# Kernel optimization log

Hardware: AMD Instinct MI355X
Metric: run time of the kernel (lower is better)

The kernel has to match this reference:

```python
import jax, jax.numpy as jnp
import numpy as np

B, L, D, H = 2, 2048, 1024, 16
HD = D // H

def setup_inputs() -> dict:
    key = jax.random.key(0)
    ks = jax.random.split(key, 5)
    s = 0.02
    return {
        "x": jax.random.normal(ks[0], (B, L, D), dtype=jnp.float32),
        "Wqkv": jax.random.normal(ks[1], (D, 3 * D), dtype=jnp.float32) * s,
        "bqkv": jnp.zeros((3 * D,), dtype=jnp.float32),
        "Wproj": jax.random.normal(ks[2], (D, D), dtype=jnp.float32) * s,
        "bproj": jnp.zeros((D,), dtype=jnp.float32),
    }

def reference(x, Wqkv, bqkv, Wproj, bproj):
    b, l, d = x.shape
    scale = (d // H) ** -0.5
    qkv = x @ Wqkv + bqkv  # (B,L,3D)
    q, k, v = jnp.split(qkv, 3, axis=-1)
    # (B,H,L,hd)
    q = q.reshape(b, l, H, HD).transpose(0, 2, 1, 3)
    k = k.reshape(b, l, H, HD).transpose(0, 2, 1, 3)
    v = v.reshape(b, l, H, HD).transpose(0, 2, 1, 3)
    attn = jnp.einsum("bhqd,bhkd->bhqk", q, k) * scale
    causal = jnp.tril(jnp.ones((l, l), dtype=bool))  # True = keep
    attn = jnp.where(causal[None, None, :, :], attn, -jnp.inf)
    attn = jax.nn.softmax(attn, axis=-1)
    out = jnp.einsum("bhqk,bhkd->bhqd", attn, v)
    out = out.transpose(0, 2, 1, 3).reshape(b, l, d)
    return out @ Wproj + bproj
```

## Files before the change

kernel.cpp:

```cpp
#include <hip/hip_runtime.h>
#include <hip/hip_bf16.h>


typedef __attribute__((ext_vector_type(8))) short s16x8;
typedef __attribute__((ext_vector_type(4))) float f32x4;

__device__ __forceinline__ unsigned short f2b(float f) {
  __hip_bfloat16 h = __float2bfloat16(f);
  return *reinterpret_cast<unsigned short*>(&h);
}

__device__ __forceinline__ void gl_lds16(const void* g, void* l) {
  __builtin_amdgcn_global_load_lds(
      (const __attribute__((address_space(1))) unsigned int*)g,
      (__attribute__((address_space(3))) unsigned int*)l,
      16, 0, 0);
}


__global__ __launch_bounds__(256) void convert_f32_bf16(
    const float* __restrict__ in, unsigned short* __restrict__ out, int n4) {
  int i = blockIdx.x * 256 + threadIdx.x;
  if (i >= n4) return;
  float4 v = reinterpret_cast<const float4*>(in)[i];
  ushort4 o;
  o.x = f2b(v.x); o.y = f2b(v.y); o.z = f2b(v.z); o.w = f2b(v.w);
  reinterpret_cast<ushort4*>(out)[i] = o;
}

__global__ __launch_bounds__(256) void transpose_f32_bf16(
    const float* __restrict__ in, unsigned short* __restrict__ out, int R, int C) {
  __shared__ float tile[32][33];
  int cb = blockIdx.x * 32, rb = blockIdx.y * 32;
  int tx = threadIdx.x, ty = threadIdx.y;
  #pragma unroll
  for (int i = ty; i < 32; i += 8)
    tile[i][tx] = in[(size_t)(rb + i) * C + cb + tx];
  __syncthreads();
  #pragma unroll
  for (int i = ty; i < 32; i += 8)
    out[(size_t)(cb + i) * R + rb + tx] = f2b(tile[tx][i]);
}

__global__ __launch_bounds__(256) void transpose_v(
    const unsigned short* __restrict__ in, unsigned short* __restrict__ out) {
  __shared__ unsigned int tile[64][65];
  const int bh = blockIdx.y;
  const int l0 = blockIdx.x * 64;
  const int tx = threadIdx.x;
  const int ty = threadIdx.y;
  #pragma unroll
  for (int i = ty; i < 64; i += 4)
    tile[i][tx] = in[((size_t)bh * 2048 + l0 + i) * 64 + tx];
  __syncthreads();
  #pragma unroll
  for (int i = ty; i < 64; i += 4)
    out[((size_t)bh * 64 + i) * 2048 + l0 + tx] = (unsigned short)tile[tx][i];
}

template <int MODE>
__global__ __launch_bounds__(256) void gemm128(
    const unsigned short* __restrict__ A, const unsigned short* __restrict__ Bt,
    const float* __restrict__ bias, unsigned short* __restrict__ qOut,
    unsigned short* __restrict__ kOut, unsigned short* __restrict__ vOut,
    float* __restrict__ fOut) {
  __shared__ char sA[16384];
  __shared__ char sB[16384];
  const int tid = threadIdx.x;
  const int wid = tid >> 6, lane = tid & 63;
  const int lg = lane >> 4, lr = lane & 15;
  const int wr = wid >> 1, wc = wid & 1;
  const int nwgx = gridDim.x;
  const int id = blockIdx.y * nwgx + blockIdx.x;
  const int cpx = (nwgx * gridDim.y) >> 3;
  const int sid = (id & 7) * cpx + (id >> 3);
  const int mb = sid / nwgx, nb = sid % nwgx;

  f32x4 acc[4][4];
  #pragma unroll
  for (int i = 0; i < 4; ++i)
    #pragma unroll
    for (int j = 0; j < 4; ++j) acc[i][j] = f32x4{0.f, 0.f, 0.f, 0.f};

  for (int ks = 0; ks < 16; ++ks) {
    __syncthreads();
    #pragma unroll
    for (int r = 0; r < 4; ++r) {
      const int chunk = r * 4 + wid;
      const int o = chunk * 1024 + lane * 16;
      const int row = o >> 7;
      const int c16 = (o >> 4) & 7;
      const int swz = (c16 ^ (row & 7)) << 4;
      gl_lds16((const char*)A + ((size_t)(mb * 128 + row) * 1024 + ks * 64) * 2 + swz,
               sA + chunk * 1024);
      gl_lds16((const char*)Bt + ((size_t)(nb * 128 + row) * 1024 + ks * 64) * 2 + swz,
               sB + chunk * 1024);
    }
    __syncthreads();
    #pragma unroll
    for (int kb = 0; kb < 2; ++kb) {
      s16x8 af[4], bfr[4];
      #pragma unroll
      for (int mt = 0; mt < 4; ++mt) {
        const int rrow = wr * 64 + mt * 16 + lr;
        const int off = kb * 64 + lg * 16;
        af[mt] = *(const s16x8*)(sA + rrow * 128 + (off ^ ((rrow & 7) << 4)));
      }
      #pragma unroll
      for (int nt = 0; nt < 4; ++nt) {
        const int rrow = wc * 64 + nt * 16 + lr;
        const int off = kb * 64 + lg * 16;
        bfr[nt] = *(const s16x8*)(sB + rrow * 128 + (off ^ ((rrow & 7) << 4)));
      }
      #pragma unroll
      for (int mt = 0; mt < 4; ++mt)
        #pragma unroll
        for (int nt = 0; nt < 4; ++nt)
          acc[mt][nt] = __builtin_amdgcn_mfma_f32_16x16x32_bf16(
              af[mt], bfr[nt], acc[mt][nt], 0, 0, 0);
    }
  }

  #pragma unroll
  for (int mt = 0; mt < 4; ++mt)
    #pragma unroll
    for (int nt = 0; nt < 4; ++nt)
      #pragma unroll
      for (int r = 0; r < 4; ++r) {
        const int m = mb * 128 + wr * 64 + mt * 16 + lg * 4 + r;
        const int n = nb * 128 + wc * 64 + nt * 16 + lr;
        float val = acc[mt][nt][r] + bias[n];
        if constexpr (MODE == 0) {
          const int b = m >> 11, ml = m & 2047;
          if (n < 1024) {
            const int h = n >> 6, d = n & 63;
            qOut[((size_t)((b * 16 + h) * 2048 + ml)) * 64 + d] =
                f2b(val * 0.18033688f);
          } else if (n < 2048) {
            const int nn = n - 1024, h = nn >> 6, d = nn & 63;
            kOut[((size_t)((b * 16 + h) * 2048 + ml)) * 64 + d] = f2b(val);
          } else {
            const int nn = n - 2048, h = nn >> 6, d = nn & 63;
            vOut[((size_t)((b * 16 + h) * 2048 + ml)) * 64 + d] = f2b(val);
          }
        } else {
          fOut[(size_t)m * 1024 + n] = val;
        }
      }
}

__global__ __launch_bounds__(256, 2) void attn_fwd(
    const unsigned short* __restrict__ Q, const unsigned short* __restrict__ Kb,
    const unsigned short* __restrict__ Vt, unsigned short* __restrict__ O) {
  __shared__ char sP[16384];
  __shared__ float obuf[32 * 68];
  __shared__ float mlbuf[4][32][2];
  __shared__ float lginv[32];

  const int bid = blockIdx.x;
  const int idx = bid >> 3;
  const int bh = (bid & 7) * 4 + (idx & 3);
  const int qseg = 63 - (idx >> 2);
  const int b = bh >> 4, h = bh & 15;
  const int tid = threadIdx.x;
  const int wid = tid >> 6, lane = tid & 63;
  const int lg = lane >> 4, lr = lane & 15;
  const int base = qseg * 32;

  for (int i = tid; i < 32 * 68; i += 256) obuf[i] = 0.f;

  s16x8 qf[2][2];
  #pragma unroll
  for (int mt = 0; mt < 2; ++mt)
    #pragma unroll
    for (int kb = 0; kb < 2; ++kb) {
      const int row = base + mt * 16 + lr;
      qf[mt][kb] = *(const s16x8*)(Q + (size_t)(bh * 2048 + row) * 64 + kb * 32 + lg * 8);
    }

  f32x4 acc[2][4];
  float rm[2][4], rl[2][4];
  #pragma unroll
  for (int i = 0; i < 2; ++i)
    #pragma unroll
    for (int jj = 0; jj < 4; ++jj) {
      acc[i][jj] = f32x4{0.f, 0.f, 0.f, 0.f};
      rm[i][jj] = -INFINITY;
      rl[i][jj] = 0.f;
    }

  char* wbase = sP + wid * 4096;
  const int nkv = (qseg >> 1) + 1;

  for (int t = wid; t < nkv; t += 4) {
    const int kv0 = t * 64;

    f32x4 sfr[2][4];
    #pragma unroll
    for (int i = 0; i < 2; ++i)
      #pragma unroll
      for (int jj = 0; jj < 4; ++jj) sfr[i][jj] = f32x4{0.f, 0.f, 0.f, 0.f};
    #pragma unroll
    for (int kb = 0; kb < 2; ++kb) {
      s16x8 kf[4];
      #pragma unroll
      for (int nt = 0; nt < 4; ++nt)
        kf[nt] = *(const s16x8*)(Kb +
            (size_t)(bh * 2048 + kv0 + nt * 16 + lr) * 64 + kb * 32 + lg * 8);
      #pragma unroll
      for (int mt = 0; mt < 2; ++mt)
        #pragma unroll
        for (int nt = 0; nt < 4; ++nt)
          sfr[mt][nt] = __builtin_amdgcn_mfma_f32_16x16x32_bf16(
              qf[mt][kb], kf[nt], sfr[mt][nt], 0, 0, 0);
    }

    s16x8 vf[2][4];
    #pragma unroll
    for (int kb = 0; kb < 2; ++kb)
      #pragma unroll
      for (int nt = 0; nt < 4; ++nt)
        vf[kb][nt] = *(const s16x8*)(Vt +
            (size_t)(bh * 64 + nt * 16 + lr) * 2048 + kv0 + kb * 32 + lg * 8);

    #pragma unroll
    for (int mt = 0; mt < 2; ++mt) {
      #pragma unroll
      for (int r = 0; r < 4; ++r) {
        const int grow = base + mt * 16 + lg * 4 + r;
        float tmax = -INFINITY;
        #pragma unroll
        for (int nt = 0; nt < 4; ++nt) {
          const int col = kv0 + nt * 16 + lr;
          float s = sfr[mt][nt][r];
          if (col > grow) s = -INFINITY;
          sfr[mt][nt][r] = s;
          tmax = fmaxf(tmax, s);
        }
        tmax = fmaxf(tmax, __shfl_xor(tmax, 1));
        tmax = fmaxf(tmax, __shfl_xor(tmax, 2));
        tmax = fmaxf(tmax, __shfl_xor(tmax, 4));
        tmax = fmaxf(tmax, __shfl_xor(tmax, 8));
        const float mold = rm[mt][r];
        const float mnew = fmaxf(mold, tmax);
        const float alpha = exp2f(mold - mnew);
        float psum = 0.f;
        #pragma unroll
        for (int nt = 0; nt < 4; ++nt) {
          const float p = exp2f(sfr[mt][nt][r] - mnew);
          sfr[mt][nt][r] = p;
          psum += p;
        }
        psum += __shfl_xor(psum, 1);
        psum += __shfl_xor(psum, 2);
        psum += __shfl_xor(psum, 4);
        psum += __shfl_xor(psum, 8);
        rl[mt][r] = rl[mt][r] * alpha + psum;
        rm[mt][r] = mnew;
        #pragma unroll
        for (int nt = 0; nt < 4; ++nt) acc[mt][nt][r] *= alpha;
        const int prow = mt * 16 + lg * 4 + r;
        #pragma unroll
        for (int nt = 0; nt < 4; ++nt) {
          const int pcolb = nt * 32 + lr * 2;
          *(unsigned short*)(wbase + prow * 128 + (pcolb ^ ((prow & 7) << 4))) =
              f2b(sfr[mt][nt][r]);
        }
      }
    }

    s16x8 pf[2][2];
    #pragma unroll
    for (int mt = 0; mt < 2; ++mt)
      #pragma unroll
      for (int kb = 0; kb < 2; ++kb) {
        const int prow = mt * 16 + lr;
        const int off = kb * 64 + lg * 16;
        pf[mt][kb] = *(const s16x8*)(wbase + prow * 128 + (off ^ ((prow & 7) << 4)));
      }
    #pragma unroll
    for (int mt = 0; mt < 2; ++mt)
      #pragma unroll
      for (int nt = 0; nt < 4; ++nt)
        #pragma unroll
        for (int kb = 0; kb < 2; ++kb)
          acc[mt][nt] = __builtin_amdgcn_mfma_f32_16x16x32_bf16(
              pf[mt][kb], vf[kb][nt], acc[mt][nt], 0, 0, 0);
  }

  if (lr == 0) {
    #pragma unroll
    for (int mt = 0; mt < 2; ++mt)
      #pragma unroll
      for (int r = 0; r < 4; ++r) {
        const int row = mt * 16 + lg * 4 + r;
        mlbuf[wid][row][0] = rm[mt][r];
        mlbuf[wid][row][1] = rl[mt][r];
      }
  }
  __syncthreads();

  float beta[2][4];
  #pragma unroll
  for (int mt = 0; mt < 2; ++mt)
    #pragma unroll
    for (int r = 0; r < 4; ++r) {
      const int row = mt * 16 + lg * 4 + r;
      const float m0 = mlbuf[0][row][0], m1 = mlbuf[1][row][0];
      const float m2 = mlbuf[2][row][0], m3 = mlbuf[3][row][0];
      const float mg = fmaxf(fmaxf(m0, m1), fmaxf(m2, m3));
      const float lsum = mlbuf[0][row][1] * exp2f(m0 - mg)
                       + mlbuf[1][row][1] * exp2f(m1 - mg)
                       + mlbuf[2][row][1] * exp2f(m2 - mg)
                       + mlbuf[3][row][1] * exp2f(m3 - mg);
      beta[mt][r] = exp2f(rm[mt][r] - mg);
      if (wid == 0 && lr == 0) lginv[row] = 1.f / lsum;
    }

  #pragma unroll
  for (int w = 0; w < 4; ++w) {
    if (wid == w) {
      #pragma unroll
      for (int mt = 0; mt < 2; ++mt)
        #pragma unroll
        for (int nt = 0; nt < 4; ++nt)
          #pragma unroll
          for (int r = 0; r < 4; ++r) {
            const int row = mt * 16 + lg * 4 + r;
            const int col = nt * 16 + lr;
            obuf[row * 68 + col] += acc[mt][nt][r] * beta[mt][r];
          }
    }
    __syncthreads();
  }

  {
    const int row = (wid << 3) + (lane >> 3);
    const int c0 = (lane & 7) * 8;
    const float li = lginv[row];
    const float4 v0 = *(const float4*)&obuf[row * 68 + c0];
    const float4 v1 = *(const float4*)&obuf[row * 68 + c0 + 4];
    s16x8 o;
    o[0] = (short)f2b(v0.x * li); o[1] = (short)f2b(v0.y * li);
    o[2] = (short)f2b(v0.z * li); o[3] = (short)f2b(v0.w * li);
    o[4] = (short)f2b(v1.x * li); o[5] = (short)f2b(v1.y * li);
    o[6] = (short)f2b(v1.z * li); o[7] = (short)f2b(v1.w * li);
    const int grow = base + row;
    *(s16x8*)(O + (size_t)(b * 2048 + grow) * 1024 + h * 64 + c0) = o;
  }
}


extern "C" void kernel_launch(void* const* d_in, const int* in_sizes, int n_in,
                              void* d_out, int out_size, void* d_ws, size_t ws_size,
                              hipStream_t stream) {
  const float* x     = (const float*)d_in[0];
  const float* Wqkv  = (const float*)d_in[1];
  const float* bqkv  = (const float*)d_in[2];
  const float* Wproj = (const float*)d_in[3];
  const float* bproj = (const float*)d_in[4];
  float* out = (float*)d_out;

  char* ws = (char*)d_ws;
  unsigned short* xb    = (unsigned short*)(ws);
  unsigned short* wqkvt = (unsigned short*)(ws + (8ull << 20));
  unsigned short* wprjt = (unsigned short*)(ws + (14ull << 20));
  unsigned short* qb    = (unsigned short*)(ws + (16ull << 20));
  unsigned short* kb    = (unsigned short*)(ws + (24ull << 20));
  unsigned short* vT    = (unsigned short*)(ws + (32ull << 20));
  unsigned short* Ob    = (unsigned short*)(ws + (40ull << 20));
  unsigned short* vtmp  = Ob;

  convert_f32_bf16<<<4096, 256, 0, stream>>>(x, xb, 1048576);
  transpose_f32_bf16<<<dim3(96, 32), dim3(32, 8), 0, stream>>>(Wqkv, wqkvt, 1024, 3072);
  transpose_f32_bf16<<<dim3(32, 32), dim3(32, 8), 0, stream>>>(Wproj, wprjt, 1024, 1024);
  gemm128<0><<<dim3(24, 32), 256, 0, stream>>>(xb, wqkvt, bqkv, qb, kb, vtmp, nullptr);
  transpose_v<<<dim3(32, 32), dim3(64, 4), 0, stream>>>(vtmp, vT);
  attn_fwd<<<2048, 256, 0, stream>>>(qb, kb, vT, Ob);
  gemm128<1><<<dim3(8, 32), 256, 0, stream>>>(Ob, wprjt, bproj, nullptr, nullptr, nullptr, out);
}
```

Measured before the change: 252.6 us.

## Use transposed 32x32 MFMA attention to keep P in registers

Rewrites the attention inner loop to compute S^T with 32x32x16 bf16 MFMAs, so each lane owns one query row. Row max and sum then reduce in-register with a single cross-half shuffle. P is packed to bf16 with v_cvt_pk_bf16_f32 and rearranged with v_permlane32_swap into the B-operand layout, which removes the LDS round trip for P. The causal mask now runs only on diagonal tiles, at the cost of relying on gfx950-specific instructions and a different register layout.

Measured after the change: 232.7 us. 7.9% less time.

```diff
diff --git a/kernel.cpp b/kernel.cpp
--- a/kernel.cpp
+++ b/kernel.cpp
@@ -4,10 +4,21 @@
 
 typedef __attribute__((ext_vector_type(8))) short s16x8;
 typedef __attribute__((ext_vector_type(4))) float f32x4;
+typedef __attribute__((ext_vector_type(16))) float f32x16;
+typedef __attribute__((ext_vector_type(4))) unsigned int u32x4;
 
 __device__ __forceinline__ unsigned short f2b(float f) {
   __hip_bfloat16 h = __float2bfloat16(f);
   return *reinterpret_cast<unsigned short*>(&h);
+}
+
+__device__ __forceinline__ unsigned int cvtpk(float a, float b) {
+  unsigned int r;
+  asm("v_cvt_pk_bf16_f32 %0, %1, %2" : "=v"(r) : "v"(a), "v"(b));
+  return r;
+}
+__device__ __forceinline__ void pl32swap(unsigned int& a, unsigned int& b) {
+  asm("v_permlane32_swap_b32 %0, %1" : "+v"(a), "+v"(b));
 }
 
 __device__ __forceinline__ void gl_lds16(const void* g, void* l) {
@@ -152,7 +163,6 @@
 __global__ __launch_bounds__(256, 2) void attn_fwd(
     const unsigned short* __restrict__ Q, const unsigned short* __restrict__ Kb,
     const unsigned short* __restrict__ Vt, unsigned short* __restrict__ O) {
-  __shared__ char sP[16384];
   __shared__ float obuf[32 * 68];
   __shared__ float mlbuf[4][32][2];
   __shared__ float lginv[32];
@@ -164,172 +174,136 @@
   const int b = bh >> 4, h = bh & 15;
   const int tid = threadIdx.x;
   const int wid = tid >> 6, lane = tid & 63;
-  const int lg = lane >> 4, lr = lane & 15;
+  const int ql = lane & 31, hi = lane >> 5;
   const int base = qseg * 32;
+  const int q = base + ql;
 
   for (int i = tid; i < 32 * 68; i += 256) obuf[i] = 0.f;
 
-  s16x8 qf[2][2];
-  #pragma unroll
-  for (int mt = 0; mt < 2; ++mt)
-    #pragma unroll
-    for (int kb = 0; kb < 2; ++kb) {
-      const int row = base + mt * 16 + lr;
-      qf[mt][kb] = *(const s16x8*)(Q + (size_t)(bh * 2048 + row) * 64 + kb * 32 + lg * 8);
-    }
-
-  f32x4 acc[2][4];
-  float rm[2][4], rl[2][4];
-  #pragma unroll
-  for (int i = 0; i < 2; ++i)
-    #pragma unroll
-    for (int jj = 0; jj < 4; ++jj) {
-      acc[i][jj] = f32x4{0.f, 0.f, 0.f, 0.f};
-      rm[i][jj] = -INFINITY;
-      rl[i][jj] = 0.f;
-    }
-
-  char* wbase = sP + wid * 4096;
+  s16x8 qf[4];
+  #pragma unroll
+  for (int ks = 0; ks < 4; ++ks)
+    qf[ks] = *(const s16x8*)(Q + (size_t)(bh * 2048 + q) * 64 + ks * 16 + hi * 8);
+
+  f32x16 acc[2];
+  #pragma unroll
+  for (int db = 0; db < 2; ++db)
+    #pragma unroll
+    for (int r = 0; r < 16; ++r) acc[db][r] = 0.f;
+  float rm = -INFINITY, rl = 0.f;
+
   const int nkv = (qseg >> 1) + 1;
 
   for (int t = wid; t < nkv; t += 4) {
     const int kv0 = t * 64;
 
-    f32x4 sfr[2][4];
-    #pragma unroll
-    for (int i = 0; i < 2; ++i)
-      #pragma unroll
-      for (int jj = 0; jj < 4; ++jj) sfr[i][jj] = f32x4{0.f, 0.f, 0.f, 0.f};
-    #pragma unroll
-    for (int kb = 0; kb < 2; ++kb) {
-      s16x8 kf[4];
-      #pragma unroll
-      for (int nt = 0; nt < 4; ++nt)
-        kf[nt] = *(const s16x8*)(Kb +
-            (size_t)(bh * 2048 + kv0 + nt * 16 + lr) * 64 + kb * 32 + lg * 8);
-      #pragma unroll
-      for (int mt = 0; mt < 2; ++mt)
+    f32x16 pt[2];
+    #pragma unroll
+    for (int kvb = 0; kvb < 2; ++kvb)
+      #pragma unroll
+      for (int r = 0; r < 16; ++r) pt[kvb][r] = 0.f;
+    #pragma unroll
+    for (int kvb = 0; kvb < 2; ++kvb)
+      #pragma unroll
+      for (int ks = 0; ks < 4; ++ks) {
+        s16x8 kf = *(const s16x8*)(Kb +
+            (size_t)(bh * 2048 + kv0 + kvb * 32 + ql) * 64 + ks * 16 + hi * 8);
+        pt[kvb] = __builtin_amdgcn_mfma_f32_32x32x16_bf16(
+            kf, qf[ks], pt[kvb], 0, 0, 0);
+      }
+
+    if (kv0 + 63 > base) {
+      #pragma unroll
+      for (int kvb = 0; kvb < 2; ++kvb)
         #pragma unroll
-        for (int nt = 0; nt < 4; ++nt)
-          sfr[mt][nt] = __builtin_amdgcn_mfma_f32_16x16x32_bf16(
-              qf[mt][kb], kf[nt], sfr[mt][nt], 0, 0, 0);
+        for (int r = 0; r < 16; ++r) {
+          const int kv = kv0 + kvb * 32 + (r & 3) + 8 * (r >> 2) + 4 * hi;
+          pt[kvb][r] = (kv > q) ? -INFINITY : pt[kvb][r];
+        }
     }
 
-    s16x8 vf[2][4];
-    #pragma unroll
-    for (int kb = 0; kb < 2; ++kb)
-      #pragma unroll
-      for (int nt = 0; nt < 4; ++nt)
-        vf[kb][nt] = *(const s16x8*)(Vt +
-            (size_t)(bh * 64 + nt * 16 + lr) * 2048 + kv0 + kb * 32 + lg * 8);
-
-    #pragma unroll
-    for (int mt = 0; mt < 2; ++mt) {
-      #pragma unroll
-      for (int r = 0; r < 4; ++r) {
-        const int grow = base + mt * 16 + lg * 4 + r;
-        float tmax = -INFINITY;
+    float tm = -INFINITY;
+    #pragma unroll
+    for (int kvb = 0; kvb < 2; ++kvb)
+      #pragma unroll
+      for (int r = 0; r < 16; ++r) tm = fmaxf(tm, pt[kvb][r]);
+    tm = fmaxf(tm, __shfl_xor(tm, 32));
+    const float mnew = fmaxf(rm, tm);
+    const float alpha = exp2f(rm - mnew);
+    float psum = 0.f;
+    #pragma unroll
+    for (int kvb = 0; kvb < 2; ++kvb)
+      #pragma unroll
+      for (int r = 0; r < 16; ++r) {
+        const float p = exp2f(pt[kvb][r] - mnew);
+        pt[kvb][r] = p;
+        psum += p;
+      }
+    psum += __shfl_xor(psum, 32);
+    rl = rl * alpha + psum;
+    rm = mnew;
+    #pragma unroll
+    for (int db = 0; db < 2; ++db)
+      #pragma unroll
+      for (int r = 0; r < 16; ++r) acc[db][r] *= alpha;
+
+    s16x8 pfrag[2][2];
+    #pragma unroll
+    for (int kvb = 0; kvb < 2; ++kvb)
+      #pragma unroll
+      for (int ks2 = 0; ks2 < 2; ++ks2) {
+        const int r0 = ks2 * 8;
+        unsigned int x = cvtpk(pt[kvb][r0 + 0], pt[kvb][r0 + 1]);
+        unsigned int y = cvtpk(pt[kvb][r0 + 2], pt[kvb][r0 + 3]);
+        unsigned int z = cvtpk(pt[kvb][r0 + 4], pt[kvb][r0 + 5]);
+        unsigned int w = cvtpk(pt[kvb][r0 + 6], pt[kvb][r0 + 7]);
+        pl32swap(x, z);
+        pl32swap(y, w);
+        u32x4 pw;
+        pw[0] = x; pw[1] = y; pw[2] = z; pw[3] = w;
+        pfrag[kvb][ks2] = __builtin_bit_cast(s16x8, pw);
+      }
+
+    #pragma unroll
+    for (int db = 0; db < 2; ++db)
+      #pragma unroll
+      for (int kvb = 0; kvb < 2; ++kvb)
         #pragma unroll
-        for (int nt = 0; nt < 4; ++nt) {
-          const int col = kv0 + nt * 16 + lr;
-          float s = sfr[mt][nt][r];
-          if (col > grow) s = -INFINITY;
-          sfr[mt][nt][r] = s;
-          tmax = fmaxf(tmax, s);
+        for (int ks2 = 0; ks2 < 2; ++ks2) {
+          s16x8 vf = *(const s16x8*)(Vt +
+              (size_t)(bh * 64 + db * 32 + ql) * 2048 +
+              kv0 + kvb * 32 + ks2 * 16 + hi * 8);
+          acc[db] = __builtin_amdgcn_mfma_f32_32x32x16_bf16(
+              vf, pfrag[kvb][ks2], acc[db], 0, 0, 0);
         }
-        tmax = fmaxf(tmax, __shfl_xor(tmax, 1));
-        tmax = fmaxf(tmax, __shfl_xor(tmax, 2));
-        tmax = fmaxf(tmax, __shfl_xor(tmax, 4));
-        tmax = fmaxf(tmax, __shfl_xor(tmax, 8));
-        const float mold = rm[mt][r];
-        const float mnew = fmaxf(mold, tmax);
-        const float alpha = exp2f(mold - mnew);
-        float psum = 0.f;
-        #pragma unroll
-        for (int nt = 0; nt < 4; ++nt) {
-          const float p = exp2f(sfr[mt][nt][r] - mnew);
-          sfr[mt][nt][r] = p;
-          psum += p;
-        }
-        psum += __shfl_xor(psum, 1);
-        psum += __shfl_xor(psum, 2);
-        psum += __shfl_xor(psum, 4);
-        psum += __shfl_xor(psum, 8);
-        rl[mt][r] = rl[mt][r] * alpha + psum;
-        rm[mt][r] = mnew;
-        #pragma unroll
-        for (int nt = 0; nt < 4; ++nt) acc[mt][nt][r] *= alpha;
-        const int prow = mt * 16 + lg * 4 + r;
-        #pragma unroll
-        for (int nt = 0; nt < 4; ++nt) {
-          const int pcolb = nt * 32 + lr * 2;
-          *(unsigned short*)(wbase + prow * 128 + (pcolb ^ ((prow & 7) << 4))) =
-              f2b(sfr[mt][nt][r]);
-        }
-      }
-    }
-
-    s16x8 pf[2][2];
-    #pragma unroll
-    for (int mt = 0; mt < 2; ++mt)
-      #pragma unroll
-      for (int kb = 0; kb < 2; ++kb) {
-        const int prow = mt * 16 + lr;
-        const int off = kb * 64 + lg * 16;
-        pf[mt][kb] = *(const s16x8*)(wbase + prow * 128 + (off ^ ((prow & 7) << 4)));
-      }
-    #pragma unroll
-    for (int mt = 0; mt < 2; ++mt)
-      #pragma unroll
-      for (int nt = 0; nt < 4; ++nt)
-        #pragma unroll
-        for (int kb = 0; kb < 2; ++kb)
-          acc[mt][nt] = __builtin_amdgcn_mfma_f32_16x16x32_bf16(
-              pf[mt][kb], vf[kb][nt], acc[mt][nt], 0, 0, 0);
-  }
-
-  if (lr == 0) {
-    #pragma unroll
-    for (int mt = 0; mt < 2; ++mt)
-      #pragma unroll
-      for (int r = 0; r < 4; ++r) {
-        const int row = mt * 16 + lg * 4 + r;
-        mlbuf[wid][row][0] = rm[mt][r];
-        mlbuf[wid][row][1] = rl[mt][r];
-      }
+  }
+
+  if (lane < 32) {
+    mlbuf[wid][ql][0] = rm;
+    mlbuf[wid][ql][1] = rl;
   }
   __syncthreads();
 
-  float beta[2][4];
-  #pragma unroll
-  for (int mt = 0; mt < 2; ++mt)
-    #pragma unroll
-    for (int r = 0; r < 4; ++r) {
-      const int row = mt * 16 + lg * 4 + r;
-      const float m0 = mlbuf[0][row][0], m1 = mlbuf[1][row][0];
-      const float m2 = mlbuf[2][row][0], m3 = mlbuf[3][row][0];
-      const float mg = fmaxf(fmaxf(m0, m1), fmaxf(m2, m3));
-      const float lsum = mlbuf[0][row][1] * exp2f(m0 - mg)
-                       + mlbuf[1][row][1] * exp2f(m1 - mg)
-                       + mlbuf[2][row][1] * exp2f(m2 - mg)
-                       + mlbuf[3][row][1] * exp2f(m3 - mg);
-      beta[mt][r] = exp2f(rm[mt][r] - mg);
-      if (wid == 0 && lr == 0) lginv[row] = 1.f / lsum;
-    }
+  const float m0 = mlbuf[0][ql][0], m1 = mlbuf[1][ql][0];
+  const float m2 = mlbuf[2][ql][0], m3 = mlbuf[3][ql][0];
+  const float mg = fmaxf(fmaxf(m0, m1), fmaxf(m2, m3));
+  const float lsum = mlbuf[0][ql][1] * exp2f(m0 - mg)
+                   + mlbuf[1][ql][1] * exp2f(m1 - mg)
+                   + mlbuf[2][ql][1] * exp2f(m2 - mg)
+                   + mlbuf[3][ql][1] * exp2f(m3 - mg);
+  const float beta = exp2f(rm - mg);
+  if (wid == 0 && lane < 32) lginv[ql] = 1.f / lsum;
 
   #pragma unroll
   for (int w = 0; w < 4; ++w) {
     if (wid == w) {
       #pragma unroll
-      for (int mt = 0; mt < 2; ++mt)
+      for (int db = 0; db < 2; ++db)
         #pragma unroll
-        for (int nt = 0; nt < 4; ++nt)
-          #pragma unroll
-          for (int r = 0; r < 4; ++r) {
-            const int row = mt * 16 + lg * 4 + r;
-            const int col = nt * 16 + lr;
-            obuf[row * 68 + col] += acc[mt][nt][r] * beta[mt][r];
-          }
+        for (int r = 0; r < 16; ++r) {
+          const int d = db * 32 + (r & 3) + 8 * (r >> 2) + 4 * hi;
+          obuf[ql * 68 + d] += acc[db][r] * beta;
+        }
     }
     __syncthreads();
   }
```
